# Optimization experiments

Hardware: AMD Instinct MI355X
Metric: run time of the kernel (lower is better)

The kernel has to match this reference:

```python
import jax, jax.numpy as jnp
import numpy as np

# dims: T tokens, E experts, D model dim, F ffn dim, C per-expert capacity, K top-k routing
T, E, D, F, C, K = 4096, 8, 1024, 4096, 1536, 2


def setup_inputs() -> dict:
    key = jax.random.key(0)
    k_x, k_lg, k_w1, k_w2 = jax.random.split(key, 4)
    x = jax.random.normal(k_x, (T, D), jnp.float32)
    # external router: top-K of logits per token, softmax weights over kept logits
    logits = jax.random.normal(k_lg, (T, E), jnp.float32)
    topv, topi = jax.lax.top_k(logits, K)                      # (T,K)
    rows = jnp.arange(T)[:, None]
    route_mask = jnp.zeros((T, E), bool).at[rows, topi].set(True)
    route_weight = jnp.zeros((T, E), jnp.float32).at[rows, topi].set(
        jax.nn.softmax(topv, axis=-1))
    # stacked homogeneous expert MLP params (E leading axis, as in _stack_group)
    W1 = jax.random.normal(k_w1, (E, D, F), jnp.float32) / np.sqrt(D)
    b1 = jnp.zeros((E, F), jnp.float32)
    W2 = jax.random.normal(k_w2, (E, F, D), jnp.float32) / np.sqrt(F)
    b2 = jnp.zeros((E, D), jnp.float32)
    return dict(x=x, route_mask=route_mask, route_weight=route_weight,
                W1=W1, b1=b1, W2=W2, b2=b2)


def reference(x, route_mask, route_weight, W1, b1, W2, b2):
    """MoE with per-expert capacity: top-C tokens per expert by route weight,
    gather -> vmapped expert MLP -> weighted scatter-combine.
    Math identical to the one-hot slot einsums ('ect,t...->ec...' dispatch and
    'ecf,ect,te->tf' combine) of the original, expressed as gather/scatter.
    """
    Tn, En = route_mask.shape
    w_te = jnp.where(route_mask, route_weight, 0.0)            # (T,E)
    # per-expert scores; unrouted tokens get -inf so they can never be selected
    w_et = jnp.where(route_mask.T, w_te.T, -jnp.inf)           # (E,T)
    vals, idx = jax.lax.top_k(w_et, C)                         # (E,C) token ids per slot
    valid = jnp.isfinite(vals)                                  # slot actually filled
    # dispatch: gather token features into (E,C,D); empty slots are zero rows
    xe = x[idx] * valid[..., None]
    # grouped expert MLP (vmap over E via batched einsum)
    h = jax.nn.relu(jnp.einsum('ecd,edf->ecf', xe, W1) + b1[:, None, :])
    out = jnp.einsum('ecf,efd->ecd', h, W2) + b2[:, None, :]    # (E,C,D)
    # combine: y[t] = sum over slots assigned to t of w_te[t,e] * out[e,c]
    gain = jnp.where(valid, jnp.take_along_axis(w_te.T, idx, axis=1), 0.0)  # (E,C)
    y = jnp.zeros((Tn, out.shape[-1]), out.dtype)
    y = y.at[idx.reshape(-1)].add((out * gain[..., None]).reshape(-1, out.shape[-1]))
    return y
```

## Files before the change

kernel.cpp:

```cpp
#include <hip/hip_runtime.h>
#include <hip/hip_bf16.h>
#include <stdint.h>

#define T_TOK 4096
#define NE    8
#define DM    1024
#define FF    4096
#define CAP   1536

typedef __attribute__((ext_vector_type(8))) __bf16 bf16x8;
typedef __attribute__((ext_vector_type(4))) float  f32x4;

__device__ __forceinline__ void gload_lds16(const void* gptr, void* lptr) {
  __builtin_amdgcn_global_load_lds(
      (__attribute__((address_space(1))) void*)(uintptr_t)gptr,
      (__attribute__((address_space(3))) void*)(uintptr_t)lptr,
      16, 0, 0);
}


__global__ void conv_x_kernel(const float4* __restrict__ src, ushort4* __restrict__ dst, int n4) {
  int i = blockIdx.x * blockDim.x + threadIdx.x;
  if (i >= n4) return;
  float4 v = src[i];
  ushort4 o;
  o.x = __builtin_bit_cast(unsigned short, __float2bfloat16(v.x));
  o.y = __builtin_bit_cast(unsigned short, __float2bfloat16(v.y));
  o.z = __builtin_bit_cast(unsigned short, __float2bfloat16(v.z));
  o.w = __builtin_bit_cast(unsigned short, __float2bfloat16(v.w));
  dst[i] = o;
}

__global__ __launch_bounds__(256)
void tconv_kernel(const float* __restrict__ src, __hip_bfloat16* __restrict__ dst,
                  int R, int C) {
  __shared__ float tile[64][65];
  const int b  = blockIdx.z;
  const int r0 = blockIdx.y * 64;
  const int c0 = blockIdx.x * 64;
  const float* s = src + (size_t)b * R * C;
  __hip_bfloat16* d = dst + (size_t)b * R * C;
  const int tid = threadIdx.x;
  const int tx = tid & 63, ty = tid >> 6;
#pragma unroll
  for (int rr = ty; rr < 64; rr += 4)
    tile[rr][tx] = s[(size_t)(r0 + rr) * C + c0 + tx];
  __syncthreads();
  const int lg = tid & 15;
  const int cg = tid >> 4;
#pragma unroll
  for (int w = 0; w < 4; ++w) {
    const int cc = w * 16 + cg;
    const int r4 = lg * 4;
    ushort4 o;
    o.x = __builtin_bit_cast(unsigned short, __float2bfloat16(tile[r4 + 0][cc]));
    o.y = __builtin_bit_cast(unsigned short, __float2bfloat16(tile[r4 + 1][cc]));
    o.z = __builtin_bit_cast(unsigned short, __float2bfloat16(tile[r4 + 2][cc]));
    o.w = __builtin_bit_cast(unsigned short, __float2bfloat16(tile[r4 + 3][cc]));
    *(ushort4*)&d[(size_t)(c0 + cc) * R + r0 + r4] = o;
  }
}

__global__ void router_kernel(const float* __restrict__ rw, int* __restrict__ counts,
                              int* __restrict__ tok_ids, float* __restrict__ gains) {
  int t = blockIdx.x * blockDim.x + threadIdx.x;
  if (t >= T_TOK) return;
#pragma unroll
  for (int e = 0; e < NE; ++e) {
    float w = rw[t * NE + e];
    if (w > 0.f) {
      int pos = atomicAdd(&counts[e], 1);
      if (pos < CAP) {
        tok_ids[e * CAP + pos] = t;
        gains[e * CAP + pos]   = w;
      }
    }
  }
}

__global__ void pad_kernel(const int* __restrict__ counts, int* __restrict__ tok_ids,
                           float* __restrict__ gains) {
  int i = blockIdx.x * blockDim.x + threadIdx.x;
  if (i >= NE * CAP) return;
  int e = i / CAP, pos = i % CAP;
  int ne = min(counts[e], CAP);
  if (pos >= ne) { tok_ids[i] = 0; gains[i] = 0.f; }
}


template <int PASS>
__global__ __launch_bounds__(256, 2)
void moe_gemm(const __hip_bfloat16* __restrict__ Asrc,
              const __hip_bfloat16* __restrict__ Bsrc,
              const float* __restrict__ bias,
              const int* __restrict__ counts,
              const int* __restrict__ tok_ids,
              const float* __restrict__ gains,
              __hip_bfloat16* __restrict__ Hout,
              float* __restrict__ y)
{
  constexpr int K  = (PASS == 1) ? DM : FF;
  constexpr int NP = (PASS == 1) ? FF : DM;
  constexpr int MT = CAP / 128;
  constexpr int NT = NP / 128;
  constexpr int KT = K / 64;

  const int bid = blockIdx.x;
  const int e   = bid / (MT * NT);
  const int rem = bid % (MT * NT);
  const int mt  = rem / NT;
  const int nt  = rem % NT;

  const int Ne = min(counts[e], CAP);
  const int m0 = mt * 128;
  if (m0 >= Ne) return;
  const int n0 = nt * 128;

  __shared__ alignas(16) __hip_bfloat16 As[128 * 64];
  __shared__ alignas(16) __hip_bfloat16 Bs[128 * 64];

  const int tid  = threadIdx.x;
  const int lane = tid & 63;
  const int wid  = tid >> 6;
  const int wm   = wid >> 1;
  const int wn   = wid & 1;

  const int srow8 = (tid >> 3) & 7;
  const int cs    = ((tid & 7) ^ srow8) * 8;

  const __hip_bfloat16 *aP[4], *bP[4];
#pragma unroll
  for (int i = 0; i < 4; ++i) {
    const int row = i * 32 + (tid >> 3);
    if (PASS == 1) {
      const int tok = tok_ids[e * CAP + m0 + row];
      aP[i] = Asrc + (size_t)tok * DM + cs;
    } else {
      aP[i] = Asrc + ((size_t)e * CAP + m0 + row) * FF + cs;
    }
    bP[i] = Bsrc + ((size_t)e * NP + n0 + row) * K + cs;
  }

  const char* AsB = (const char*)As;
  const char* BsB = (const char*)Bs;
  const int fr = lane & 15;
  const int fq = lane >> 4;
  const int kb0 = ((fq + 0) ^ (fr & 7)) << 4;
  const int kb1 = ((fq + 4) ^ (fr & 7)) << 4;

  f32x4 acc[4][4] = {};

  for (int kt = 0; kt < KT; ++kt) {
#pragma unroll
    for (int i = 0; i < 4; ++i)
      gload_lds16(aP[i] + kt * 64, (char*)As + i * 4096 + tid * 16);
#pragma unroll
    for (int i = 0; i < 4; ++i)
      gload_lds16(bP[i] + kt * 64, (char*)Bs + i * 4096 + tid * 16);
    __syncthreads();

#pragma unroll
    for (int s = 0; s < 2; ++s) {
      const int kb = s ? kb1 : kb0;
      bf16x8 af[4], bfr[4];
#pragma unroll
      for (int i = 0; i < 4; ++i)
        af[i] = *(const bf16x8*)(AsB + (wm * 64 + i * 16 + fr) * 128 + kb);
#pragma unroll
      for (int j = 0; j < 4; ++j)
        bfr[j] = *(const bf16x8*)(BsB + (wn * 64 + j * 16 + fr) * 128 + kb);
#pragma unroll
      for (int i = 0; i < 4; ++i)
#pragma unroll
        for (int j = 0; j < 4; ++j)
          acc[i][j] = __builtin_amdgcn_mfma_f32_16x16x32_bf16(af[i], bfr[j], acc[i][j], 0, 0, 0);
    }
    __syncthreads();
  }

  const int colb = n0 + wn * 64 + fr;
  if (PASS == 1) {
#pragma unroll
    for (int j = 0; j < 4; ++j) {
      const float bv = bias[(size_t)e * NP + colb + j * 16];
#pragma unroll
      for (int i = 0; i < 4; ++i)
#pragma unroll
        for (int rr = 0; rr < 4; ++rr) {
          const int row = m0 + wm * 64 + i * 16 + fq * 4 + rr;
          float v = acc[i][j][rr] + bv;
          v = v > 0.f ? v : 0.f;
          Hout[((size_t)e * CAP + row) * FF + colb + j * 16] = __float2bfloat16(v);
        }
    }
  } else {
    float bv[4];
#pragma unroll
    for (int j = 0; j < 4; ++j) bv[j] = bias[(size_t)e * NP + colb + j * 16];
#pragma unroll
    for (int i = 0; i < 4; ++i)
#pragma unroll
      for (int rr = 0; rr < 4; ++rr) {
        const int row  = m0 + wm * 64 + i * 16 + fq * 4 + rr;
        const int slot = e * CAP + row;
        const float g  = gains[slot];
        if (g != 0.f) {
          const int tok = tok_ids[slot];
          float* yrow = y + (size_t)tok * DM + colb;
#pragma unroll
          for (int j = 0; j < 4; ++j)
            atomicAdd(yrow + j * 16, (acc[i][j][rr] + bv[j]) * g);
        }
      }
  }
}


extern "C" void kernel_launch(void* const* d_in, const int* in_sizes, int n_in,
                              void* d_out, int out_size, void* d_ws, size_t ws_size,
                              hipStream_t stream) {
  const float* x  = (const float*)d_in[0];
  const float* rw = (const float*)d_in[2];
  const float* W1 = (const float*)d_in[3];
  const float* b1 = (const float*)d_in[4];
  const float* W2 = (const float*)d_in[5];
  const float* b2 = (const float*)d_in[6];
  float* y = (float*)d_out;

  char* ws = (char*)d_ws;
  size_t off = 0;
  auto alloc = [&](size_t bytes) {
    void* p = ws + off;
    off = (off + bytes + 255) & ~(size_t)255;
    return p;
  };
  __hip_bfloat16* xb  = (__hip_bfloat16*)alloc((size_t)T_TOK * DM * 2);
  __hip_bfloat16* w1t = (__hip_bfloat16*)alloc((size_t)NE * DM * FF * 2);
  __hip_bfloat16* w2t = (__hip_bfloat16*)alloc((size_t)NE * FF * DM * 2);
  __hip_bfloat16* Hb  = (__hip_bfloat16*)alloc((size_t)NE * CAP * FF * 2);
  int*   counts  = (int*)alloc(NE * sizeof(int));
  int*   tok_ids = (int*)alloc((size_t)NE * CAP * sizeof(int));
  float* gains   = (float*)alloc((size_t)NE * CAP * sizeof(float));
  (void)ws_size; (void)in_sizes; (void)n_in; (void)out_size;

  hipMemsetAsync(y, 0, (size_t)T_TOK * DM * sizeof(float), stream);
  hipMemsetAsync(counts, 0, NE * sizeof(int), stream);

  conv_x_kernel<<<(T_TOK * DM / 4 + 255) / 256, 256, 0, stream>>>(
      (const float4*)x, (ushort4*)xb, T_TOK * DM / 4);
  tconv_kernel<<<dim3(FF / 64, DM / 64, NE), 256, 0, stream>>>(W1, w1t, DM, FF);
  tconv_kernel<<<dim3(DM / 64, FF / 64, NE), 256, 0, stream>>>(W2, w2t, FF, DM);
  router_kernel<<<(T_TOK + 255) / 256, 256, 0, stream>>>(rw, counts, tok_ids, gains);
  pad_kernel<<<(NE * CAP + 255) / 256, 256, 0, stream>>>(counts, tok_ids, gains);

  moe_gemm<1><<<NE * (CAP / 128) * (FF / 128), 256, 0, stream>>>(
      xb, w1t, b1, counts, tok_ids, gains, Hb, nullptr);
  moe_gemm<2><<<NE * (CAP / 128) * (DM / 128), 256, 0, stream>>>(
      Hb, w2t, b2, counts, tok_ids, gains, nullptr, y);
}
```

Before: 323.7 us.

## Widen first expert GEMM tile to 128x256 with 512 threads; fold padding into memset

Result: slower. 335.3 us (+3.6%).

```diff
diff --git a/kernel.cpp b/kernel.cpp
--- a/kernel.cpp
+++ b/kernel.cpp
@@ -78,31 +78,19 @@
   }
 }
 
-__global__ void pad_kernel(const int* __restrict__ counts, int* __restrict__ tok_ids,
-                           float* __restrict__ gains) {
-  int i = blockIdx.x * blockDim.x + threadIdx.x;
-  if (i >= NE * CAP) return;
-  int e = i / CAP, pos = i % CAP;
-  int ne = min(counts[e], CAP);
-  if (pos >= ne) { tok_ids[i] = 0; gains[i] = 0.f; }
-}
-
-
-template <int PASS>
-__global__ __launch_bounds__(256, 2)
-void moe_gemm(const __hip_bfloat16* __restrict__ Asrc,
-              const __hip_bfloat16* __restrict__ Bsrc,
-              const float* __restrict__ bias,
-              const int* __restrict__ counts,
-              const int* __restrict__ tok_ids,
-              const float* __restrict__ gains,
-              __hip_bfloat16* __restrict__ Hout,
-              float* __restrict__ y)
+
+__global__ __launch_bounds__(512, 2)
+void moe_gemm_p1(const __hip_bfloat16* __restrict__ xb,
+                 const __hip_bfloat16* __restrict__ w1t,
+                 const float* __restrict__ bias,
+                 const int* __restrict__ counts,
+                 const int* __restrict__ tok_ids,
+                 __hip_bfloat16* __restrict__ Hout)
 {
-  constexpr int K  = (PASS == 1) ? DM : FF;
-  constexpr int NP = (PASS == 1) ? FF : DM;
+  constexpr int K  = DM;
+  constexpr int NP = FF;
   constexpr int MT = CAP / 128;
-  constexpr int NT = NP / 128;
+  constexpr int NT = NP / 256;
   constexpr int KT = K / 64;
 
   const int bid = blockIdx.x;
@@ -114,32 +102,29 @@
   const int Ne = min(counts[e], CAP);
   const int m0 = mt * 128;
   if (m0 >= Ne) return;
-  const int n0 = nt * 128;
+  const int n0 = nt * 256;
 
   __shared__ alignas(16) __hip_bfloat16 As[128 * 64];
-  __shared__ alignas(16) __hip_bfloat16 Bs[128 * 64];
+  __shared__ alignas(16) __hip_bfloat16 Bs[256 * 64];
 
   const int tid  = threadIdx.x;
   const int lane = tid & 63;
   const int wid  = tid >> 6;
-  const int wm   = wid >> 1;
-  const int wn   = wid & 1;
-
-  const int srow8 = (tid >> 3) & 7;
-  const int cs    = ((tid & 7) ^ srow8) * 8;
-
-  const __hip_bfloat16 *aP[4], *bP[4];
-#pragma unroll
-  for (int i = 0; i < 4; ++i) {
-    const int row = i * 32 + (tid >> 3);
-    if (PASS == 1) {
-      const int tok = tok_ids[e * CAP + m0 + row];
-      aP[i] = Asrc + (size_t)tok * DM + cs;
-    } else {
-      aP[i] = Asrc + ((size_t)e * CAP + m0 + row) * FF + cs;
-    }
-    bP[i] = Bsrc + ((size_t)e * NP + n0 + row) * K + cs;
-  }
+  const int wm   = wid >> 2;
+  const int wn   = wid & 3;
+
+  const int srow = tid >> 3;
+  const int cs   = ((tid & 7) ^ (srow & 7)) * 8;
+
+  const __hip_bfloat16 *aP[2], *bP[4];
+#pragma unroll
+  for (int i = 0; i < 2; ++i) {
+    const int tok = tok_ids[e * CAP + m0 + i * 64 + srow];
+    aP[i] = xb + (size_t)tok * DM + cs;
+  }
+#pragma unroll
+  for (int i = 0; i < 4; ++i)
+    bP[i] = w1t + ((size_t)e * NP + n0 + i * 64 + srow) * K + cs;
 
   const char* AsB = (const char*)As;
   const char* BsB = (const char*)Bs;
@@ -152,11 +137,11 @@
 
   for (int kt = 0; kt < KT; ++kt) {
 #pragma unroll
+    for (int i = 0; i < 2; ++i)
+      gload_lds16(aP[i] + kt * 64, (char*)As + i * 8192 + tid * 16);
+#pragma unroll
     for (int i = 0; i < 4; ++i)
-      gload_lds16(aP[i] + kt * 64, (char*)As + i * 4096 + tid * 16);
-#pragma unroll
-    for (int i = 0; i < 4; ++i)
-      gload_lds16(bP[i] + kt * 64, (char*)Bs + i * 4096 + tid * 16);
+      gload_lds16(bP[i] + kt * 64, (char*)Bs + i * 8192 + tid * 16);
     __syncthreads();
 
 #pragma unroll
@@ -179,40 +164,124 @@
   }
 
   const int colb = n0 + wn * 64 + fr;
-  if (PASS == 1) {
-#pragma unroll
-    for (int j = 0; j < 4; ++j) {
-      const float bv = bias[(size_t)e * NP + colb + j * 16];
+#pragma unroll
+  for (int j = 0; j < 4; ++j) {
+    const float bv = bias[(size_t)e * NP + colb + j * 16];
+#pragma unroll
+    for (int i = 0; i < 4; ++i)
+#pragma unroll
+      for (int rr = 0; rr < 4; ++rr) {
+        const int row = m0 + wm * 64 + i * 16 + fq * 4 + rr;
+        float v = acc[i][j][rr] + bv;
+        v = v > 0.f ? v : 0.f;
+        Hout[((size_t)e * CAP + row) * FF + colb + j * 16] = __float2bfloat16(v);
+      }
+  }
+}
+
+
+__global__ __launch_bounds__(256, 2)
+void moe_gemm_p2(const __hip_bfloat16* __restrict__ Hb,
+                 const __hip_bfloat16* __restrict__ w2t,
+                 const float* __restrict__ bias,
+                 const int* __restrict__ counts,
+                 const int* __restrict__ tok_ids,
+                 const float* __restrict__ gains,
+                 float* __restrict__ y)
+{
+  constexpr int K  = FF;
+  constexpr int NP = DM;
+  constexpr int MT = CAP / 128;
+  constexpr int NT = NP / 128;
+  constexpr int KT = K / 64;
+
+  const int bid = blockIdx.x;
+  const int e   = bid / (MT * NT);
+  const int rem = bid % (MT * NT);
+  const int mt  = rem / NT;
+  const int nt  = rem % NT;
+
+  const int Ne = min(counts[e], CAP);
+  const int m0 = mt * 128;
+  if (m0 >= Ne) return;
+  const int n0 = nt * 128;
+
+  __shared__ alignas(16) __hip_bfloat16 As[128 * 64];
+  __shared__ alignas(16) __hip_bfloat16 Bs[128 * 64];
+
+  const int tid  = threadIdx.x;
+  const int lane = tid & 63;
+  const int wid  = tid >> 6;
+  const int wm   = wid >> 1;
+  const int wn   = wid & 1;
+
+  const int srow8 = (tid >> 3) & 7;
+  const int cs    = ((tid & 7) ^ srow8) * 8;
+
+  const __hip_bfloat16 *aP[4], *bP[4];
+#pragma unroll
+  for (int i = 0; i < 4; ++i) {
+    const int row = i * 32 + (tid >> 3);
+    aP[i] = Hb + ((size_t)e * CAP + m0 + row) * FF + cs;
+    bP[i] = w2t + ((size_t)e * NP + n0 + row) * K + cs;
+  }
+
+  const char* AsB = (const char*)As;
+  const char* BsB = (const char*)Bs;
+  const int fr = lane & 15;
+  const int fq = lane >> 4;
+  const int kb0 = ((fq + 0) ^ (fr & 7)) << 4;
+  const int kb1 = ((fq + 4) ^ (fr & 7)) << 4;
+
+  f32x4 acc[4][4] = {};
+
+  for (int kt = 0; kt < KT; ++kt) {
+#pragma unroll
+    for (int i = 0; i < 4; ++i)
+      gload_lds16(aP[i] + kt * 64, (char*)As + i * 4096 + tid * 16);
+#pragma unroll
+    for (int i = 0; i < 4; ++i)
+      gload_lds16(bP[i] + kt * 64, (char*)Bs + i * 4096 + tid * 16);
+    __syncthreads();
+
+#pragma unroll
+    for (int s = 0; s < 2; ++s) {
+      const int kb = s ? kb1 : kb0;
+      bf16x8 af[4], bfr[4];
 #pragma unroll
       for (int i = 0; i < 4; ++i)
-#pragma unroll
-        for (int rr = 0; rr < 4; ++rr) {
-          const int row = m0 + wm * 64 + i * 16 + fq * 4 + rr;
-          float v = acc[i][j][rr] + bv;
-          v = v > 0.f ? v : 0.f;
-          Hout[((size_t)e * CAP + row) * FF + colb + j * 16] = __float2bfloat16(v);
-        }
+        af[i] = *(const bf16x8*)(AsB + (wm * 64 + i * 16 + fr) * 128 + kb);
+#pragma unroll
+      for (int j = 0; j < 4; ++j)
+        bfr[j] = *(const bf16x8*)(BsB + (wn * 64 + j * 16 + fr) * 128 + kb);
+#pragma unroll
+      for (int i = 0; i < 4; ++i)
+#pragma unroll
+        for (int j = 0; j < 4; ++j)
+          acc[i][j] = __builtin_amdgcn_mfma_f32_16x16x32_bf16(af[i], bfr[j], acc[i][j], 0, 0, 0);
     }
-  } else {
-    float bv[4];
-#pragma unroll
-    for (int j = 0; j < 4; ++j) bv[j] = bias[(size_t)e * NP + colb + j * 16];
-#pragma unroll
-    for (int i = 0; i < 4; ++i)
-#pragma unroll
-      for (int rr = 0; rr < 4; ++rr) {
-        const int row  = m0 + wm * 64 + i * 16 + fq * 4 + rr;
-        const int slot = e * CAP + row;
-        const float g  = gains[slot];
-        if (g != 0.f) {
-          const int tok = tok_ids[slot];
-          float* yrow = y + (size_t)tok * DM + colb;
-#pragma unroll
-          for (int j = 0; j < 4; ++j)
-            atomicAdd(yrow + j * 16, (acc[i][j][rr] + bv[j]) * g);
-        }
+    __syncthreads();
+  }
+
+  const int colb = n0 + wn * 64 + fr;
+  float bv[4];
+#pragma unroll
+  for (int j = 0; j < 4; ++j) bv[j] = bias[(size_t)e * NP + colb + j * 16];
+#pragma unroll
+  for (int i = 0; i < 4; ++i)
+#pragma unroll
+    for (int rr = 0; rr < 4; ++rr) {
+      const int row  = m0 + wm * 64 + i * 16 + fq * 4 + rr;
+      const int slot = e * CAP + row;
+      const float g  = gains[slot];
+      if (g != 0.f) {
+        const int tok = tok_ids[slot];
+        float* yrow = y + (size_t)tok * DM + colb;
+#pragma unroll
+        for (int j = 0; j < 4; ++j)
+          atomicAdd(yrow + j * 16, (acc[i][j][rr] + bv[j]) * g);
       }
-  }
+    }
 }
 
 
@@ -244,17 +313,17 @@
   (void)ws_size; (void)in_sizes; (void)n_in; (void)out_size;
 
   hipMemsetAsync(y, 0, (size_t)T_TOK * DM * sizeof(float), stream);
-  hipMemsetAsync(counts, 0, NE * sizeof(int), stream);
+  const size_t ctl_bytes = (size_t)((char*)(gains + NE * CAP) - (char*)counts);
+  hipMemsetAsync(counts, 0, ctl_bytes, stream);
 
   conv_x_kernel<<<(T_TOK * DM / 4 + 255) / 256, 256, 0, stream>>>(
       (const float4*)x, (ushort4*)xb, T_TOK * DM / 4);
   tconv_kernel<<<dim3(FF / 64, DM / 64, NE), 256, 0, stream>>>(W1, w1t, DM, FF);
   tconv_kernel<<<dim3(DM / 64, FF / 64, NE), 256, 0, stream>>>(W2, w2t, FF, DM);
   router_kernel<<<(T_TOK + 255) / 256, 256, 0, stream>>>(rw, counts, tok_ids, gains);
-  pad_kernel<<<(NE * CAP + 255) / 256, 256, 0, stream>>>(counts, tok_ids, gains);
-
-  moe_gemm<1><<<NE * (CAP / 128) * (FF / 128), 256, 0, stream>>>(
-      xb, w1t, b1, counts, tok_ids, gains, Hb, nullptr);
-  moe_gemm<2><<<NE * (CAP / 128) * (DM / 128), 256, 0, stream>>>(
-      Hb, w2t, b2, counts, tok_ids, gains, nullptr, y);
-}
+
+  moe_gemm_p1<<<NE * (CAP / 128) * (FF / 256), 512, 0, stream>>>(
+      xb, w1t, b1, counts, tok_ids, Hb);
+  moe_gemm_p2<<<NE * (CAP / 128) * (DM / 128), 256, 0, stream>>>(
+      Hb, w2t, b2, counts, tok_ids, gains, y);
+}
```

## Double-buffer B tile and prefetch next K-step during MFMA; drop pad kernel

Applied to the files above, without the earlier changes.

Result: slower. 351.7 us (+8.7%).

```diff
diff --git a/kernel.cpp b/kernel.cpp
--- a/kernel.cpp
+++ b/kernel.cpp
@@ -78,18 +78,9 @@
   }
 }
 
-__global__ void pad_kernel(const int* __restrict__ counts, int* __restrict__ tok_ids,
-                           float* __restrict__ gains) {
-  int i = blockIdx.x * blockDim.x + threadIdx.x;
-  if (i >= NE * CAP) return;
-  int e = i / CAP, pos = i % CAP;
-  int ne = min(counts[e], CAP);
-  if (pos >= ne) { tok_ids[i] = 0; gains[i] = 0.f; }
-}
-
 
 template <int PASS>
-__global__ __launch_bounds__(256, 2)
+__global__ __launch_bounds__(256)
 void moe_gemm(const __hip_bfloat16* __restrict__ Asrc,
               const __hip_bfloat16* __restrict__ Bsrc,
               const float* __restrict__ bias,
@@ -116,8 +107,7 @@
   if (m0 >= Ne) return;
   const int n0 = nt * 128;
 
-  __shared__ alignas(16) __hip_bfloat16 As[128 * 64];
-  __shared__ alignas(16) __hip_bfloat16 Bs[128 * 64];
+  __shared__ alignas(16) char LDSb[49152];
 
   const int tid  = threadIdx.x;
   const int lane = tid & 63;
@@ -141,8 +131,6 @@
     bP[i] = Bsrc + ((size_t)e * NP + n0 + row) * K + cs;
   }
 
-  const char* AsB = (const char*)As;
-  const char* BsB = (const char*)Bs;
   const int fr = lane & 15;
   const int fq = lane >> 4;
   const int kb0 = ((fq + 0) ^ (fr & 7)) << 4;
@@ -150,33 +138,56 @@
 
   f32x4 acc[4][4] = {};
 
+#define STAGE_A(kt) do {                                                       \
+    _Pragma("unroll") for (int i = 0; i < 4; ++i)                              \
+      gload_lds16(aP[i] + (kt) * 64, LDSb + i * 4096 + tid * 16);              \
+  } while (0)
+#define STAGE_B(buf, kt) do {                                                  \
+    _Pragma("unroll") for (int i = 0; i < 4; ++i)                              \
+      gload_lds16(bP[i] + (kt) * 64,                                           \
+                  LDSb + 16384 + (buf) * 16384 + i * 4096 + tid * 16);         \
+  } while (0)
+
+  STAGE_A(0);
+  STAGE_B(0, 0);
+
+#pragma unroll 1
   for (int kt = 0; kt < KT; ++kt) {
-#pragma unroll
-    for (int i = 0; i < 4; ++i)
-      gload_lds16(aP[i] + kt * 64, (char*)As + i * 4096 + tid * 16);
-#pragma unroll
-    for (int i = 0; i < 4; ++i)
-      gload_lds16(bP[i] + kt * 64, (char*)Bs + i * 4096 + tid * 16);
     __syncthreads();
 
+    bf16x8 areg[2][4];
 #pragma unroll
     for (int s = 0; s < 2; ++s) {
       const int kb = s ? kb1 : kb0;
-      bf16x8 af[4], bfr[4];
 #pragma unroll
       for (int i = 0; i < 4; ++i)
-        af[i] = *(const bf16x8*)(AsB + (wm * 64 + i * 16 + fr) * 128 + kb);
+        areg[s][i] = *(const bf16x8*)(LDSb + (wm * 64 + i * 16 + fr) * 128 + kb);
+    }
+    __syncthreads();
+
+    if (kt + 1 < KT) {
+      STAGE_A(kt + 1);
+      STAGE_B((kt + 1) & 1, kt + 1);
+    }
+
+    const char* Bb = LDSb + 16384 + (kt & 1) * 16384;
+#pragma unroll
+    for (int s = 0; s < 2; ++s) {
+      const int kb = s ? kb1 : kb0;
+      bf16x8 bfr[4];
 #pragma unroll
       for (int j = 0; j < 4; ++j)
-        bfr[j] = *(const bf16x8*)(BsB + (wn * 64 + j * 16 + fr) * 128 + kb);
+        bfr[j] = *(const bf16x8*)(Bb + (wn * 64 + j * 16 + fr) * 128 + kb);
 #pragma unroll
       for (int i = 0; i < 4; ++i)
 #pragma unroll
         for (int j = 0; j < 4; ++j)
-          acc[i][j] = __builtin_amdgcn_mfma_f32_16x16x32_bf16(af[i], bfr[j], acc[i][j], 0, 0, 0);
-    }
-    __syncthreads();
-  }
+          acc[i][j] = __builtin_amdgcn_mfma_f32_16x16x32_bf16(areg[s][i], bfr[j], acc[i][j], 0, 0, 0);
+    }
+  }
+
+#undef STAGE_A
+#undef STAGE_B
 
   const int colb = n0 + wn * 64 + fr;
   if (PASS == 1) {
@@ -244,14 +255,14 @@
   (void)ws_size; (void)in_sizes; (void)n_in; (void)out_size;
 
   hipMemsetAsync(y, 0, (size_t)T_TOK * DM * sizeof(float), stream);
-  hipMemsetAsync(counts, 0, NE * sizeof(int), stream);
+  const size_t ctl_bytes = (size_t)((char*)(gains + NE * CAP) - (char*)counts);
+  hipMemsetAsync(counts, 0, ctl_bytes, stream);
 
   conv_x_kernel<<<(T_TOK * DM / 4 + 255) / 256, 256, 0, stream>>>(
       (const float4*)x, (ushort4*)xb, T_TOK * DM / 4);
   tconv_kernel<<<dim3(FF / 64, DM / 64, NE), 256, 0, stream>>>(W1, w1t, DM, FF);
   tconv_kernel<<<dim3(DM / 64, FF / 64, NE), 256, 0, stream>>>(W2, w2t, FF, DM);
   router_kernel<<<(T_TOK + 255) / 256, 256, 0, stream>>>(rw, counts, tok_ids, gains);
-  pad_kernel<<<(NE * CAP + 255) / 256, 256, 0, stream>>>(counts, tok_ids, gains);
 
   moe_gemm<1><<<NE * (CAP / 128) * (FF / 128), 256, 0, stream>>>(
       xb, w1t, b1, counts, tok_ids, gains, Hb, nullptr);
```
